# Performance work log

Hardware: AMD Instinct MI355X
Metric: run time of the kernel (lower is better)

## Reference

```python
import jax, jax.numpy as jnp
import numpy as np

B, N, C, K = 8, 4096, 64, 16
MLP = [64, 64, 128]
IN_CH = C * 2 + 3  # 131
EPS = 1e-5


def setup_inputs() -> dict:
    key = jax.random.key(0)
    ks = jax.random.split(key, 16)
    inp = {
        "pos1": jax.random.normal(ks[0], (B, 3, N), jnp.float32),
        "pos1_re": jax.random.normal(ks[1], (B, 3, N), jnp.float32),
        "pos2": jax.random.normal(ks[2], (B, 3, N), jnp.float32),
        "feature1": jax.random.normal(ks[3], (B, C, N), jnp.float32),
        "feature2": jax.random.normal(ks[4], (B, C, N), jnp.float32),
        "ksample": K,
    }
    # 1x1 Conv2d weights (out, in), no bias; BN affine params per layer
    last = IN_CH
    for i, out in enumerate(MLP):
        inp[f"W{i}"] = jax.random.normal(ks[5 + i], (out, last), jnp.float32) * (1.0 / np.sqrt(last))
        inp[f"g{i}"] = 1.0 + 0.1 * jax.random.normal(ks[8 + i], (out,), jnp.float32)
        inp[f"b{i}"] = 0.1 * jax.random.normal(ks[11 + i], (out,), jnp.float32)
        last = out
    return inp


def _knn_idx(query, ref, k):
    # query: [B,N,3], ref: [B,M,3] -> idx [B,N,k] of nearest refs per query
    q2 = jnp.sum(query * query, -1, keepdims=True)          # [B,N,1]
    r2 = jnp.sum(ref * ref, -1)[:, None, :]                 # [B,1,M]
    d = q2 + r2 - 2.0 * jnp.einsum("bnc,bmc->bnm", query, ref)
    _, idx = jax.lax.top_k(-d, k)
    return idx


def _group(x, idx):
    # x: [B,Cx,M], idx: [B,N,k] -> [B,Cx,N,k]
    xt = jnp.transpose(x, (0, 2, 1))                         # [B,M,Cx]
    g = jax.vmap(lambda a, i: a[i])(xt, idx)                 # [B,N,k,Cx]
    return jnp.transpose(g, (0, 3, 1, 2))


def _bn_relu(x, g, b):
    # training-mode BatchNorm2d over (B,N,k) per channel, then ReLU
    mean = jnp.mean(x, axis=(0, 2, 3), keepdims=True)
    var = jnp.mean((x - mean) ** 2, axis=(0, 2, 3), keepdims=True)
    xh = (x - mean) * jax.lax.rsqrt(var + EPS)
    return jax.nn.relu(xh * g[None, :, None, None] + b[None, :, None, None])


def reference(pos1, pos1_re, pos2, feature1, feature2, ksample,
              W0, g0, b0, W1, g1, b1, W2, g2, b2):
    idx = _knn_idx(jnp.transpose(pos1_re, (0, 2, 1)),
                   jnp.transpose(pos2, (0, 2, 1)), ksample)   # [B,N,k]
    pos2_g = _group(pos2, idx)                                # [B,3,N,k]
    pos_diff = pos2_g - pos1[:, :, :, None]
    feat2_g = _group(feature2, idx)                           # [B,C,N,k]
    feat1_rep = jnp.broadcast_to(feature1[:, :, :, None], feat2_g.shape)
    x = jnp.concatenate([pos_diff, feat2_g, feat1_rep], axis=1)  # [B,2C+3,N,k]
    for W, g, b in ((W0, g0, b0), (W1, g1, b1), (W2, g2, b2)):
        x = _bn_relu(jnp.einsum("oc,bcnk->bonk", W, x), g, b)
    feat1_new = jnp.max(x, axis=-1)                           # [B,mlp[-1],N]
    return pos1, feat1_new
```

## Files before the change

### kernel.cpp

```cpp
#include <hip/hip_runtime.h>
#include <hip/hip_bf16.h>
#include <cstdint>
#include <cstddef>

#define BB   8
#define NN   4096
#define CC   64
#define KK   16
#define H2   128
#define NPOSF 524288.0f
#define BNEPS 1e-5f

typedef __attribute__((ext_vector_type(8))) short  short8;
typedef __attribute__((ext_vector_type(4))) float  f32x4;

#define MFMA(a,b,c) __builtin_amdgcn_mfma_f32_16x16x32_bf16(a, b, c, 0, 0, 0)

__device__ __forceinline__ unsigned short f2bf(float x) {
  union { float f; unsigned u; } v; v.f = x;
  unsigned u = v.u;
  return (unsigned short)((u + 0x7fffu + ((u >> 16) & 1u)) >> 16);
}
__device__ __forceinline__ float bf2f(unsigned short h) {
  union { unsigned u; float f; } v; v.u = ((unsigned)h) << 16; return v.f;
}
__device__ __forceinline__ unsigned long long shflxor64(unsigned long long v, int j) {
  unsigned lo = (unsigned)v, hi = (unsigned)(v >> 32);
  lo = (unsigned)__shfl_xor((int)lo, j);
  hi = (unsigned)__shfl_xor((int)hi, j);
  return ((unsigned long long)hi << 32) | lo;
}
__device__ __forceinline__ unsigned long long shfl64(unsigned long long v, int src) {
  unsigned lo = (unsigned)v, hi = (unsigned)(v >> 32);
  lo = (unsigned)__shfl((int)lo, src);
  hi = (unsigned)__shfl((int)hi, src);
  return ((unsigned long long)hi << 32) | lo;
}

#define BN_INLINE(S_, Q_, g_, b_, aLds, bLds, CH) \
  if (t < CH) { \
    float s = 0.f, qq = 0.f; \
    for (int c = 0; c < 32; ++c) { s += S_[c*CH + t]; qq += Q_[c*CH + t]; } \
    float mean = s * (1.0f / NPOSF); \
    float var  = qq * (1.0f / NPOSF) - mean*mean; \
    float rs   = 1.0f / sqrtf(var + BNEPS); \
    float a    = g_[t] * rs; \
    aLds[t] = a; bLds[t] = b_[t] - mean*a; \
  }

__global__ __launch_bounds__(256) void k_prep(const float* __restrict__ pos2, float4* __restrict__ out,
                                              const float* __restrict__ pos1, float* __restrict__ outP,
                                              float* __restrict__ stats) {
  int i = blockIdx.x * 256 + threadIdx.x;
  int b = i >> 12, n = i & 4095;
  float x = pos2[(b*3 + 0)*NN + n];
  float y = pos2[(b*3 + 1)*NN + n];
  float z = pos2[(b*3 + 2)*NN + n];
  float w = __fadd_rn(__fadd_rn(__fmul_rn(x,x), __fmul_rn(y,y)), __fmul_rn(z,z));
  out[i] = make_float4(x, y, z, w);
  if (i < BB*3*NN/4) {
    *(float4*)(outP + i*4) = *(const float4*)(pos1 + i*4);
  }
  if (i < 16384) stats[i] = 0.f;
}

__global__ __launch_bounds__(256) void k_transposeb2(const float* __restrict__ f2, const float* __restrict__ f1,
                                                     unsigned short* __restrict__ o2, unsigned short* __restrict__ o1) {
  __shared__ float tile[32][33];
  int z = blockIdx.z;
  int b = z & 7;
  const float* in = (z < 8) ? f2 : f1;
  unsigned short* out = (z < 8) ? o2 : o1;
  int n0 = blockIdx.x * 32, c0 = blockIdx.y * 32;
  int tx = threadIdx.x, ty = threadIdx.y;
  #pragma unroll
  for (int i = 0; i < 32; i += 8)
    tile[ty + i][tx] = in[((size_t)(b*CC + c0 + ty + i))*NN + n0 + tx];
  __syncthreads();
  #pragma unroll
  for (int i = 0; i < 32; i += 8)
    out[((size_t)(b*NN + n0 + ty + i))*CC + c0 + tx] = f2bf(tile[tx][ty + i]);
}

__global__ __launch_bounds__(256) void k_wt(const float* __restrict__ W0, const float* __restrict__ W1,
                                            const float* __restrict__ W2, unsigned short* __restrict__ Apk0,
                                            unsigned short* __restrict__ Apk1, unsigned short* __restrict__ Apk2) {
  int i = blockIdx.x * 256 + threadIdx.x;
  if (i < 1280) {
    int mt = i / 320, r = i % 320, s = r / 64, lane = r % 64;
    int o = mt*16 + (lane & 15), q = lane >> 4, fi = mt*5 + s;
    #pragma unroll
    for (int j = 0; j < 8; ++j) {
      int c = s*32 + q*8 + j;
      float w = 0.f;
      if (c < 131) { int cs = (c < 128) ? (c + 3) : (c - 128); w = W0[o*131 + cs]; }
      Apk0[((size_t)(fi)*64 + lane)*8 + j] = f2bf(w);
    }
  } else if (i < 1792) {
    int k = i - 1280, mt = k / 128, r = k % 128, s = r / 64, lane = r % 64;
    int o = mt*16 + (lane & 15), q = lane >> 4, fi = mt*2 + s;
    #pragma unroll
    for (int j = 0; j < 8; ++j) {
      int c = s*32 + q*8 + j;
      Apk1[((size_t)(fi)*64 + lane)*8 + j] = f2bf(W1[o*64 + c]);
    }
  } else if (i < 2816) {
    int k = i - 1792, mt = k / 128, r = k % 128, s = r / 64, lane = r % 64;
    int o = mt*16 + (lane & 15), q = lane >> 4, fi = mt*2 + s;
    #pragma unroll
    for (int j = 0; j < 8; ++j) {
      int c = s*32 + q*8 + j;
      Apk2[((size_t)(fi)*64 + lane)*8 + j] = f2bf(W2[o*64 + c]);
    }
  }
}

__global__ __launch_bounds__(256) void k_packAB(const float* __restrict__ pos1_re,
                                                const float4* __restrict__ pos2t,
                                                unsigned short* __restrict__ ApkQ,
                                                unsigned short* __restrict__ BpkR) {
  int i = blockIdx.x * 256 + threadIdx.x;
  int half = i >> 17;
  int ii = i & 131071;
  int b = ii >> 14, r = ii & 16383;
  int qt = r >> 6, lane = r & 63;
  int li = lane & 15, g = lane >> 4;
  int n = qt*16 + li;
  if (half == 0) {
    float q[3];
    q[0] = pos1_re[(b*3 + 0)*NN + n];
    q[1] = pos1_re[(b*3 + 1)*NN + n];
    q[2] = pos1_re[(b*3 + 2)*NN + n];
    unsigned short qhi[3], qlo[3];
    #pragma unroll
    for (int c = 0; c < 3; ++c) {
      qhi[c] = f2bf(q[c]);
      qlo[c] = f2bf(__fsub_rn(q[c], bf2f(qhi[c])));
    }
    #pragma unroll
    for (int j = 0; j < 8; ++j) {
      int k = g*8 + j;
      unsigned short v = 0;
      if (k < 3)       v = qhi[k];
      else if (k < 6)  v = qhi[k-3];
      else if (k < 9)  v = qlo[k-6];
      else if (k < 11) v = 0x3F80;
      ApkQ[(((size_t)b*256 + qt)*64 + lane)*8 + j] = v;
    }
  } else {
    float4 rr = pos2t[(size_t)b*NN + n];
    float rc[3] = {rr.x, rr.y, rr.z};
    unsigned short m2hi[3], m2lo[3];
    #pragma unroll
    for (int c = 0; c < 3; ++c) {
      unsigned short rhi = f2bf(rc[c]);
      float rhif = bf2f(rhi);
      m2hi[c] = f2bf(-2.f * rhif);
      unsigned short rlo = f2bf(__fsub_rn(rc[c], rhif));
      m2lo[c] = f2bf(-2.f * bf2f(rlo));
    }
    float r2 = rr.w;
    unsigned short r2hi = f2bf(r2);
    unsigned short r2lo = f2bf(__fsub_rn(r2, bf2f(r2hi)));
    #pragma unroll
    for (int j = 0; j < 8; ++j) {
      int k = g*8 + j;
      unsigned short v = 0;
      if (k < 3)       v = m2hi[k];
      else if (k < 6)  v = m2lo[k-3];
      else if (k < 9)  v = m2hi[k-6];
      else if (k == 9) v = r2hi;
      else if (k == 10)v = r2lo;
      BpkR[(((size_t)b*256 + qt)*64 + lane)*8 + j] = v;
    }
  }
}

__global__ __launch_bounds__(512, 8) void k_knnf(const float* __restrict__ pos1_re,
                                                 const float4* __restrict__ pos2t,
                                                 const unsigned short* __restrict__ ApkQ,
                                                 const unsigned short* __restrict__ BpkR,
                                                 unsigned short* __restrict__ idxOut) {
  __shared__ unsigned short lists[16*128];
  __shared__ unsigned cnts[16];
  __shared__ float smin[16][128];
  __shared__ float thr[16][2];
  const int t = threadIdx.x, lane = t & 63, wv = t >> 6;
  const int b = blockIdx.y;
  const int qt = blockIdx.x;
  const int li = lane & 15, g = lane >> 4;

  if (t < 16) cnts[t] = 0;

  short8 af = *(const short8*)(ApkQ + (((size_t)b*256 + qt)*64 + lane)*8);
  const unsigned short* bq = BpkR + (size_t)b*256*512 + lane*8;

  const f32x4 zero4 = {0,0,0,0};

  float mn[4] = {3e38f, 3e38f, 3e38f, 3e38f};
  const int off = qt & 3;
  #pragma unroll
  for (int s = 0; s < 8; ++s) {
    short8 bf = *(const short8*)(bq + (size_t)(wv*32 + s*4 + off)*512);
    f32x4 a = MFMA(af, bf, zero4);
    #pragma unroll
    for (int rg = 0; rg < 4; ++rg) mn[rg] = fminf(mn[rg], a[rg]);
  }
  #pragma unroll
  for (int rg = 0; rg < 4; ++rg) smin[g*4 + rg][wv*16 + li] = mn[rg];
  __syncthreads();

  #pragma unroll 1
  for (int c = 0; c < 2; ++c) {
    const int rr = wv*2 + c;
    float v = fminf(smin[rr][lane], smin[rr][64 + lane]);
    #pragma unroll
    for (int k = 2; k <= 64; k <<= 1)
      #pragma unroll
      for (int j = k>>1; j > 0; j >>= 1) {
        float p = __shfl_xor(v, j);
        bool keepMin = (((lane & j) == 0) == ((lane & k) == 0));
        float mn_ = fminf(v, p), mx_ = fmaxf(v, p);
        v = keepMin ? mn_ : mx_;
      }
    float t10 = __shfl(v, 9);
    if (lane == 0) {
      const int n = qt*16 + rr;
      float qx = pos1_re[(b*3 + 0)*NN + n];
      float qy = pos1_re[(b*3 + 1)*NN + n];
      float qz = pos1_re[(b*3 + 2)*NN + n];
      float q2 = __fadd_rn(__fadd_rn(__fmul_rn(qx,qx), __fmul_rn(qy,qy)), __fmul_rn(qz,qz));
      float eps2 = __fmaf_rn(1.25e-4f, q2 + 64.f, 6e-4f);
      thr[rr][0] = t10;
      thr[rr][1] = t10 + eps2;
    }
  }
  __syncthreads();
  float tsr[4], twr[4];
  #pragma unroll
  for (int rg = 0; rg < 4; ++rg) { tsr[rg] = thr[g*4 + rg][0]; twr[rg] = thr[g*4 + rg][1]; }

  #pragma unroll 8
  for (int s = 0; s < 32; ++s) {
    const int rt = wv*32 + s;
    short8 bf = *(const short8*)(bq + (size_t)rt*512);
    f32x4 a = MFMA(af, bf, zero4);
    bool any = (a[0] < twr[0]) | (a[1] < twr[1]) | (a[2] < twr[2]) | (a[3] < twr[3]);
    if (__ballot(any)) {
      #pragma unroll
      for (int rg = 0; rg < 4; ++rg) {
        if (a[rg] < twr[rg]) {
          unsigned add = (a[rg] < tsr[rg]) ? 1u : 0x10001u;
          unsigned prev = atomicAdd(&cnts[g*4 + rg], add);
          unsigned pos = prev & 0xffffu;
          if (pos < 128u) lists[((g*4 + rg) << 7) | pos] = (unsigned short)((rt << 4) | li);
        }
      }
    }
  }
  __syncthreads();

  const float4* rp = pos2t + (size_t)b*NN;
  #pragma unroll 1
  for (int c = 0; c < 2; ++c) {
    const int qi = wv*2 + c;
    const int n = qt*16 + qi;
    unsigned cw = cnts[qi];
    unsigned cnt = cw & 0xffffu;
    int c0q = (int)cnt - (int)(cw >> 16);

    const float qx = pos1_re[(b*3 + 0)*NN + n];
    const float qy = pos1_re[(b*3 + 1)*NN + n];
    const float qz = pos1_re[(b*3 + 2)*NN + n];
    const float q2 = __fadd_rn(__fadd_rn(__fmul_rn(qx,qx), __fmul_rn(qy,qy)), __fmul_rn(qz,qz));

    if (c0q >= 16 && cnt <= 128u) {
      const unsigned short* lst = &lists[qi << 7];
      unsigned long long key = ~0ull;
      if (lane < (int)cnt) {
        int ix = lst[lane];
        float4 r = rp[ix];
        float dot = __fadd_rn(__fadd_rn(__fmul_rn(qx,r.x), __fmul_rn(qy,r.y)), __fmul_rn(qz,r.z));
        float d   = __fsub_rn(__fadd_rn(q2, r.w), __fmul_rn(2.0f, dot));
        unsigned du = __float_as_uint(d);
        du ^= (du >> 31) ? 0xFFFFFFFFu : 0x80000000u;
        key = ((unsigned long long)du << 16) | (unsigned)ix;
      }
      #pragma unroll
      for (int k = 2; k <= 64; k <<= 1)
        #pragma unroll
        for (int j = k>>1; j > 0; j >>= 1) {
          unsigned long long p = shflxor64(key, j);
          bool keepMin = (((lane & j) == 0) == ((lane & k) == 0));
          unsigned long long mnk = key < p ? key : p, mxk = key < p ? p : key;
          key = keepMin ? mnk : mxk;
        }
      if (cnt > 64u) {
        unsigned long long k2 = ~0ull;
        if (lane + 64 < (int)cnt) {
          int ix = lst[64 + lane];
          float4 r = rp[ix];
          float dot = __fadd_rn(__fadd_rn(__fmul_rn(qx,r.x), __fmul_rn(qy,r.y)), __fmul_rn(qz,r.z));
          float d   = __fsub_rn(__fadd_rn(q2, r.w), __fmul_rn(2.0f, dot));
          unsigned du = __float_as_uint(d);
          du ^= (du >> 31) ? 0xFFFFFFFFu : 0x80000000u;
          k2 = ((unsigned long long)du << 16) | (unsigned)ix;
        }
        #pragma unroll
        for (int k = 2; k <= 64; k <<= 1)
          #pragma unroll
          for (int j = k>>1; j > 0; j >>= 1) {
            unsigned long long p = shflxor64(k2, j);
            bool keepMin = (((lane & j) == 0) == ((lane & k) == 0));
            unsigned long long mnk = k2 < p ? k2 : p, mxk = k2 < p ? p : k2;
            k2 = keepMin ? mnk : mxk;
          }
        unsigned long long pb = shfl64(k2, (15 - lane) & 63);
        key = key < pb ? key : pb;
      }
      if (lane < 16) idxOut[((size_t)(b*NN + n))*KK + lane] = (unsigned short)(key & 0xffffull);
    } else {
      unsigned bd  = 0xFFFFFFFFu;
      unsigned bix = 0u;
      unsigned tau = 0xFFFFFFFFu;
      for (int it = 0; it < 64; ++it) {
        float4 r = rp[it*64 + lane];
        float dot = __fadd_rn(__fadd_rn(__fmul_rn(qx,r.x), __fmul_rn(qy,r.y)), __fmul_rn(qz,r.z));
        float d   = __fsub_rn(__fadd_rn(q2, r.w), __fmul_rn(2.0f, dot));
        unsigned du = __float_as_uint(d);
        du ^= (du >> 31) ? 0xFFFFFFFFu : 0x80000000u;
        unsigned long long mask = __ballot(du < tau);
        while (mask) {
          const int l = __ffsll((unsigned long long)mask) - 1;
          mask &= (mask - 1);
          const unsigned sd = (unsigned)__builtin_amdgcn_readlane((int)du, l);
          if (sd >= tau) continue;
          const unsigned sidx = (unsigned)(it*64 + l);
          int m = (bd > sd) ? 1 : 0;
          int pm = __builtin_amdgcn_update_dpp(0, m, 0x111, 0xF, 0xF, true);
          unsigned sb = (unsigned)__builtin_amdgcn_update_dpp(0, (int)bd,  0x111, 0xF, 0xF, true);
          unsigned si = (unsigned)__builtin_amdgcn_update_dpp(0, (int)bix, 0x111, 0xF, 0xF, true);
          if (m) { bd = pm ? sb : sd; bix = pm ? si : sidx; }
          tau = (unsigned)__builtin_amdgcn_readlane((int)bd, 15);
        }
      }
      if (lane < 16) idxOut[((size_t)(b*NN + n))*KK + lane] = (unsigned short)bix;
    }
  }
}

#define WAVE_STATS(NMT) { \
  _Pragma("unroll") \
  for (int mt = 0; mt < NMT; ++mt) { \
    _Pragma("unroll") \
    for (int rg = 0; rg < 4; ++rg) { \
      float s_ = sacc[mt][rg], q_ = sqacc[mt][rg]; \
      s_ += __shfl_xor(s_,1); s_ += __shfl_xor(s_,2); s_ += __shfl_xor(s_,4); s_ += __shfl_xor(s_,8); \
      q_ += __shfl_xor(q_,1); q_ += __shfl_xor(q_,2); q_ += __shfl_xor(q_,4); q_ += __shfl_xor(q_,8); \
      if (cl == 0) { atomicAdd(&sS[mt*16 + q*4 + rg], s_); atomicAdd(&sQ[mt*16 + q*4 + rg], q_); } \
    } \
  } }

__global__ __launch_bounds__(256) void k_layer0(
    const unsigned short* __restrict__ nidx, const float4* __restrict__ pos2t,
    const float* __restrict__ pos1, const unsigned short* __restrict__ f2b,
    const unsigned short* __restrict__ f1b, const unsigned short* __restrict__ Apk0,
    unsigned short* __restrict__ Y0, float* __restrict__ gS, float* __restrict__ gQ) {
  __shared__ float sS[64], sQ[64];
  const int t = threadIdx.x, lane = t & 63, wv = t >> 6;
  const int b = blockIdx.x & 7, xt = blockIdx.x >> 3;
  const int n0 = xt*32 + wv*8;
  const int cl = lane & 15, q = lane >> 4;

  short8 Wr[20];
  #pragma unroll
  for (int f = 0; f < 20; ++f) Wr[f] = *(const short8*)(Apk0 + ((size_t)f*64 + lane)*8);
  if (t < 64) { sS[t] = 0.f; sQ[t] = 0.f; }
  __syncthreads();

  f32x4 sacc[4]  = {{0,0,0,0},{0,0,0,0},{0,0,0,0},{0,0,0,0}};
  f32x4 sqacc[4] = {{0,0,0,0},{0,0,0,0},{0,0,0,0},{0,0,0,0}};

  #pragma unroll 1
  for (int p = 0; p < 8; ++p) {
    const int n = n0 + p;
    const int m = (int)nidx[((size_t)(b*NN + n))*KK + cl];
    const unsigned short* f2r = f2b + ((size_t)(b*NN + m))*64;
    const unsigned short* f1r = f1b + ((size_t)(b*NN + n))*64;
    short8 x0 = *(const short8*)(f2r + q*8);
    short8 x1 = *(const short8*)(f2r + 32 + q*8);
    short8 x2 = *(const short8*)(f1r + q*8);
    short8 x3 = *(const short8*)(f1r + 32 + q*8);
    short8 x4 = {0,0,0,0,0,0,0,0};
    if (q == 0) {
      float4 pp = pos2t[(size_t)b*NN + m];
      float px = pos1[(b*3 + 0)*NN + n];
      float py = pos1[(b*3 + 1)*NN + n];
      float pz = pos1[(b*3 + 2)*NN + n];
      x4[0] = (short)f2bf(pp.x - px);
      x4[1] = (short)f2bf(pp.y - py);
      x4[2] = (short)f2bf(pp.z - pz);
    }
    f32x4 acc[4] = {{0,0,0,0},{0,0,0,0},{0,0,0,0},{0,0,0,0}};
    #pragma unroll
    for (int mt = 0; mt < 4; ++mt) {
      acc[mt] = MFMA(Wr[mt*5 + 0], x0, acc[mt]);
      acc[mt] = MFMA(Wr[mt*5 + 1], x1, acc[mt]);
      acc[mt] = MFMA(Wr[mt*5 + 2], x2, acc[mt]);
      acc[mt] = MFMA(Wr[mt*5 + 3], x3, acc[mt]);
      acc[mt] = MFMA(Wr[mt*5 + 4], x4, acc[mt]);
    }
    unsigned short* yr = Y0 + (((size_t)(b*NN + n))*KK + cl)*64;
    #pragma unroll
    for (int mt = 0; mt < 4; ++mt) {
      sacc[mt]  += acc[mt];
      sqacc[mt] += acc[mt]*acc[mt];
      ushort4 pk; pk.x = f2bf(acc[mt][0]); pk.y = f2bf(acc[mt][1]);
      pk.z = f2bf(acc[mt][2]); pk.w = f2bf(acc[mt][3]);
      *(ushort4*)(yr + mt*16 + q*4) = pk;
    }
  }
  WAVE_STATS(4)
  __syncthreads();
  const int slot = xt & 31;
  if (t < 64) { atomicAdd(&gS[slot*64 + t], sS[t]); atomicAdd(&gQ[slot*64 + t], sQ[t]); }
}

__global__ __launch_bounds__(256) void k_layer1(
    const unsigned short* __restrict__ Y0, const float* __restrict__ S0, const float* __restrict__ Q0,
    const float* __restrict__ g0, const float* __restrict__ b0,
    const unsigned short* __restrict__ Apk1, unsigned short* __restrict__ Y1,
    float* __restrict__ gS, float* __restrict__ gQ) {
  __shared__ float sS[64], sQ[64];
  __shared__ float aL[64], bL[64];
  const int t = threadIdx.x, lane = t & 63, wv = t >> 6;
  const int b = blockIdx.y, n0 = blockIdx.x*32 + wv*8;
  const int cl = lane & 15, q = lane >> 4;

  short8 Wr[8];
  #pragma unroll
  for (int f = 0; f < 8; ++f) Wr[f] = *(const short8*)(Apk1 + ((size_t)f*64 + lane)*8);
  BN_INLINE(S0, Q0, g0, b0, aL, bL, 64)
  if (t >= 64 && t < 128) { sS[t-64] = 0.f; sQ[t-64] = 0.f; }
  __syncthreads();

  float ar[16], br[16];
  #pragma unroll
  for (int s = 0; s < 2; ++s)
    #pragma unroll
    for (int j = 0; j < 8; ++j) { int c = s*32 + q*8 + j; ar[s*8+j] = aL[c]; br[s*8+j] = bL[c]; }

  f32x4 sacc[4]  = {{0,0,0,0},{0,0,0,0},{0,0,0,0},{0,0,0,0}};
  f32x4 sqacc[4] = {{0,0,0,0},{0,0,0,0},{0,0,0,0},{0,0,0,0}};

  #pragma unroll 1
  for (int p = 0; p < 8; ++p) {
    const int n = n0 + p;
    const unsigned short* yr = Y0 + (((size_t)(b*NN + n))*KK + cl)*64;
    short8 u0 = *(const short8*)(yr + q*8);
    short8 u1 = *(const short8*)(yr + 32 + q*8);
    short8 x0, x1;
    #pragma unroll
    for (int j = 0; j < 8; ++j) {
      x0[j] = (short)f2bf(fmaxf(bf2f((unsigned short)u0[j])*ar[j]   + br[j],   0.f));
      x1[j] = (short)f2bf(fmaxf(bf2f((unsigned short)u1[j])*ar[8+j] + br[8+j], 0.f));
    }
    f32x4 acc[4] = {{0,0,0,0},{0,0,0,0},{0,0,0,0},{0,0,0,0}};
    #pragma unroll
    for (int mt = 0; mt < 4; ++mt) {
      acc[mt] = MFMA(Wr[mt*2 + 0], x0, acc[mt]);
      acc[mt] = MFMA(Wr[mt*2 + 1], x1, acc[mt]);
    }
    unsigned short* yw = Y1 + (((size_t)(b*NN + n))*KK + cl)*64;
    #pragma unroll
    for (int mt = 0; mt < 4; ++mt) {
      sacc[mt]  += acc[mt];
      sqacc[mt] += acc[mt]*acc[mt];
      ushort4 pk; pk.x = f2bf(acc[mt][0]); pk.y = f2bf(acc[mt][1]);
      pk.z = f2bf(acc[mt][2]); pk.w = f2bf(acc[mt][3]);
      *(ushort4*)(yw + mt*16 + q*4) = pk;
    }
  }
  WAVE_STATS(4)
  __syncthreads();
  const int slot = blockIdx.x & 31;
  if (t < 64) { atomicAdd(&gS[slot*64 + t], sS[t]); atomicAdd(&gQ[slot*64 + t], sQ[t]); }
}

__global__ __launch_bounds__(256) void k_l2stats(
    const unsigned short* __restrict__ Y1, const float* __restrict__ S1, const float* __restrict__ Q1,
    const float* __restrict__ g1, const float* __restrict__ b1,
    const unsigned short* __restrict__ Apk2, float2* __restrict__ Ypk,
    float* __restrict__ gS, float* __restrict__ gQ) {
  __shared__ float sS[128], sQ[128];
  __shared__ float aL[64], bL[64];
  const int t = threadIdx.x, lane = t & 63, wv = t >> 6;
  const int b = blockIdx.y, n0 = blockIdx.x*32 + wv*8;
  const int cl = lane & 15, q = lane >> 4;

  short8 Wr[16];
  #pragma unroll
  for (int f = 0; f < 16; ++f) Wr[f] = *(const short8*)(Apk2 + ((size_t)f*64 + lane)*8);
  BN_INLINE(S1, Q1, g1, b1, aL, bL, 64)
  if (t >= 64 && t < 192) { sS[t-64] = 0.f; sQ[t-64] = 0.f; }
  __syncthreads();

  float ar[16], br[16];
  #pragma unroll
  for (int s = 0; s < 2; ++s)
    #pragma unroll
    for (int j = 0; j < 8; ++j) { int c = s*32 + q*8 + j; ar[s*8+j] = aL[c]; br[s*8+j] = bL[c]; }

  float ssum[8] = {0,0,0,0,0,0,0,0};
  float sqsum[8] = {0,0,0,0,0,0,0,0};

  #pragma unroll 1
  for (int p = 0; p < 8; ++p) {
    const int n = n0 + p;
    const unsigned short* yr = Y1 + (((size_t)(b*NN + n))*KK + cl)*64;
    short8 u0 = *(const short8*)(yr + q*8);
    short8 u1 = *(const short8*)(yr + 32 + q*8);
    short8 x0, x1;
    #pragma unroll
    for (int j = 0; j < 8; ++j) {
      x0[j] = (short)f2bf(fmaxf(bf2f((unsigned short)u0[j])*ar[j]   + br[j],   0.f));
      x1[j] = (short)f2bf(fmaxf(bf2f((unsigned short)u1[j])*ar[8+j] + br[8+j], 0.f));
    }
    float2* yw = Ypk + ((size_t)(b*NN + n))*H2;
    #pragma unroll
    for (int mt = 0; mt < 8; ++mt) {
      f32x4 acc = {0,0,0,0};
      acc = MFMA(x0, Wr[mt*2 + 0], acc);
      acc = MFMA(x1, Wr[mt*2 + 1], acc);
      ssum[mt]  += (acc[0] + acc[1]) + (acc[2] + acc[3]);
      sqsum[mt] += acc[0]*acc[0] + acc[1]*acc[1] + acc[2]*acc[2] + acc[3]*acc[3];
      float mx = fmaxf(fmaxf(acc[0], acc[1]), fmaxf(acc[2], acc[3]));
      float mn = fminf(fminf(acc[0], acc[1]), fminf(acc[2], acc[3]));
      mx = fmaxf(mx, __shfl_xor(mx, 16)); mx = fmaxf(mx, __shfl_xor(mx, 32));
      mn = fminf(mn, __shfl_xor(mn, 16)); mn = fminf(mn, __shfl_xor(mn, 32));
      if (lane < 16) yw[mt*16 + lane] = make_float2(mx, mn);
    }
  }
  #pragma unroll
  for (int mt = 0; mt < 8; ++mt) {
    float s_ = ssum[mt], q_ = sqsum[mt];
    s_ += __shfl_xor(s_, 16); s_ += __shfl_xor(s_, 32);
    q_ += __shfl_xor(q_, 16); q_ += __shfl_xor(q_, 32);
    if (lane < 16) { atomicAdd(&sS[mt*16 + cl], s_); atomicAdd(&sQ[mt*16 + cl], q_); }
  }
  __syncthreads();
  const int slot = blockIdx.x & 31;
  if (t < 128) { atomicAdd(&gS[slot*128 + t], sS[t]); atomicAdd(&gQ[slot*128 + t], sQ[t]); }
}

__global__ __launch_bounds__(256) void k_bnmax(
    const float2* __restrict__ Ypk, const float* __restrict__ S2, const float* __restrict__ Q2,
    const float* __restrict__ g2, const float* __restrict__ b2,
    float* __restrict__ outF) {
  __shared__ float a2s[128], b2s[128];
  __shared__ float oBuf[32*128];
  const int t = threadIdx.x;
  const int b = blockIdx.y, nb = blockIdx.x*32;
  BN_INLINE(S2, Q2, g2, b2, a2s, b2s, 128)
  __syncthreads();

  const float2* src = Ypk + ((size_t)(b*NN + nb))*H2;
  #pragma unroll
  for (int e = 0; e < 16; ++e) {
    int i = e*256 + t;
    float2 v = src[i];
    int ch = i & 127;
    float a = a2s[ch];
    float sel = (a >= 0.f) ? v.x : v.y;
    oBuf[i] = fmaxf(sel*a + b2s[ch], 0.f);
  }
  __syncthreads();
  {
    const int ch = t & 127, npb = (t >> 7) * 16;
    #pragma unroll
    for (int g = 0; g < 4; ++g) {
      float4 v = make_float4(oBuf[(npb + g*4 + 0)*128 + ch],
                             oBuf[(npb + g*4 + 1)*128 + ch],
                             oBuf[(npb + g*4 + 2)*128 + ch],
                             oBuf[(npb + g*4 + 3)*128 + ch]);
      *(float4*)(outF + ((size_t)(b*H2 + ch))*NN + nb + npb + g*4) = v;
    }
  }
}

extern "C" void kernel_launch(void* const* d_in, const int* in_sizes, int n_in,
                              void* d_out, int out_size, void* d_ws, size_t ws_size,
                              hipStream_t stream) {
  const float* pos1    = (const float*)d_in[0];
  const float* pos1_re = (const float*)d_in[1];
  const float* pos2    = (const float*)d_in[2];
  const float* f1      = (const float*)d_in[3];
  const float* f2      = (const float*)d_in[4];
  const float* W0 = (const float*)d_in[6];
  const float* g0 = (const float*)d_in[7];
  const float* b0 = (const float*)d_in[8];
  const float* W1 = (const float*)d_in[9];
  const float* g1 = (const float*)d_in[10];
  const float* b1 = (const float*)d_in[11];
  const float* W2 = (const float*)d_in[12];
  const float* g2 = (const float*)d_in[13];
  const float* b2 = (const float*)d_in[14];
  float* out = (float*)d_out;

  char* ws = (char*)d_ws;
  float* stats = (float*)ws;
  float* S0 = stats;         float* Q0 = stats + 2048;
  float* S1 = stats + 4096;  float* Q1 = stats + 6144;
  float* S2 = stats + 8192;  float* Q2 = stats + 12288;
  unsigned short* Apk0 = (unsigned short*)(ws + 67584);
  unsigned short* Apk1 = (unsigned short*)(ws + 108544);
  unsigned short* Apk2 = (unsigned short*)(ws + 124928);
  unsigned short* idxb = (unsigned short*)(ws + 157696);
  float4* pos2t        = (float4*)(ws + 1206272);
  unsigned short* f2b  = (unsigned short*)(ws + 1730560);
  unsigned short* f1b  = (unsigned short*)(ws + 5924864);
  unsigned short* Y0   = (unsigned short*)(ws + 10119168);
  unsigned short* Y1   = (unsigned short*)(ws + 77228032);
  unsigned short* ApkQ = (unsigned short*)(ws + 10119168);
  unsigned short* BpkR = (unsigned short*)(ws + 10119168 + 2097152);
  float2* Ypk          = (float2*)(ws + 10119168);
  if (ws_size < 144336896u) return;

  k_wt<<<dim3(11), 256, 0, stream>>>(W0, W1, W2, Apk0, Apk1, Apk2);
  k_prep<<<dim3(BB*NN/256), 256, 0, stream>>>(pos2, pos2t, pos1, out, stats);
  k_packAB<<<dim3(1024), 256, 0, stream>>>(pos1_re, pos2t, ApkQ, BpkR);
  k_transposeb2<<<dim3(NN/32, CC/32, 2*BB), dim3(32, 8), 0, stream>>>(f2, f1, f2b, f1b);
  k_knnf<<<dim3(256, BB), 512, 0, stream>>>(pos1_re, pos2t, ApkQ, BpkR, idxb);

  k_layer0<<<dim3(NN/32*BB), 256, 0, stream>>>(idxb, pos2t, pos1, f2b, f1b, Apk0, Y0, S0, Q0);
  k_layer1<<<dim3(NN/32, BB), 256, 0, stream>>>(Y0, S0, Q0, g0, b0, Apk1, Y1, S1, Q1);
  k_l2stats<<<dim3(NN/32, BB), 256, 0, stream>>>(Y1, S1, Q1, g1, b1, Apk2, Ypk, S2, Q2);
  k_bnmax<<<dim3(NN/32, BB), 256, 0, stream>>>(Ypk, S2, Q2, g2, b2, out + (size_t)BB*3*NN);
}
```

Measured before the change: 310.6 us.

## Merge prep/pack kernels and interleave feature transpose blocks into kNN launch

Combines k_prep and k_packAB into one launch, with the pack half reading pos2 directly and recomputing the squared norm so it no longer depends on pos2t. The feature transpose work is folded into the kNN kernel as odd-numbered blocks, so the memory-bound transpose runs alongside the MFMA-heavy kNN blocks. This removes two kernel launches and their serialization gaps. In exchange the merged kNN kernel holds a shared union of LDS, and transpose blocks use 512 threads under a 512-thread launch bound.

```diff
diff --git a/kernel.cpp b/kernel.cpp
--- a/kernel.cpp
+++ b/kernel.cpp
@@ -48,78 +48,28 @@
     aLds[t] = a; bLds[t] = b_[t] - mean*a; \
   }
 
-__global__ __launch_bounds__(256) void k_prep(const float* __restrict__ pos2, float4* __restrict__ out,
-                                              const float* __restrict__ pos1, float* __restrict__ outP,
-                                              float* __restrict__ stats) {
-  int i = blockIdx.x * 256 + threadIdx.x;
-  int b = i >> 12, n = i & 4095;
-  float x = pos2[(b*3 + 0)*NN + n];
-  float y = pos2[(b*3 + 1)*NN + n];
-  float z = pos2[(b*3 + 2)*NN + n];
-  float w = __fadd_rn(__fadd_rn(__fmul_rn(x,x), __fmul_rn(y,y)), __fmul_rn(z,z));
-  out[i] = make_float4(x, y, z, w);
-  if (i < BB*3*NN/4) {
-    *(float4*)(outP + i*4) = *(const float4*)(pos1 + i*4);
-  }
-  if (i < 16384) stats[i] = 0.f;
-}
-
-__global__ __launch_bounds__(256) void k_transposeb2(const float* __restrict__ f2, const float* __restrict__ f1,
-                                                     unsigned short* __restrict__ o2, unsigned short* __restrict__ o1) {
-  __shared__ float tile[32][33];
-  int z = blockIdx.z;
-  int b = z & 7;
-  const float* in = (z < 8) ? f2 : f1;
-  unsigned short* out = (z < 8) ? o2 : o1;
-  int n0 = blockIdx.x * 32, c0 = blockIdx.y * 32;
-  int tx = threadIdx.x, ty = threadIdx.y;
-  #pragma unroll
-  for (int i = 0; i < 32; i += 8)
-    tile[ty + i][tx] = in[((size_t)(b*CC + c0 + ty + i))*NN + n0 + tx];
-  __syncthreads();
-  #pragma unroll
-  for (int i = 0; i < 32; i += 8)
-    out[((size_t)(b*NN + n0 + ty + i))*CC + c0 + tx] = f2bf(tile[tx][ty + i]);
-}
-
-__global__ __launch_bounds__(256) void k_wt(const float* __restrict__ W0, const float* __restrict__ W1,
-                                            const float* __restrict__ W2, unsigned short* __restrict__ Apk0,
-                                            unsigned short* __restrict__ Apk1, unsigned short* __restrict__ Apk2) {
-  int i = blockIdx.x * 256 + threadIdx.x;
-  if (i < 1280) {
-    int mt = i / 320, r = i % 320, s = r / 64, lane = r % 64;
-    int o = mt*16 + (lane & 15), q = lane >> 4, fi = mt*5 + s;
-    #pragma unroll
-    for (int j = 0; j < 8; ++j) {
-      int c = s*32 + q*8 + j;
-      float w = 0.f;
-      if (c < 131) { int cs = (c < 128) ? (c + 3) : (c - 128); w = W0[o*131 + cs]; }
-      Apk0[((size_t)(fi)*64 + lane)*8 + j] = f2bf(w);
-    }
-  } else if (i < 1792) {
-    int k = i - 1280, mt = k / 128, r = k % 128, s = r / 64, lane = r % 64;
-    int o = mt*16 + (lane & 15), q = lane >> 4, fi = mt*2 + s;
-    #pragma unroll
-    for (int j = 0; j < 8; ++j) {
-      int c = s*32 + q*8 + j;
-      Apk1[((size_t)(fi)*64 + lane)*8 + j] = f2bf(W1[o*64 + c]);
-    }
-  } else if (i < 2816) {
-    int k = i - 1792, mt = k / 128, r = k % 128, s = r / 64, lane = r % 64;
-    int o = mt*16 + (lane & 15), q = lane >> 4, fi = mt*2 + s;
-    #pragma unroll
-    for (int j = 0; j < 8; ++j) {
-      int c = s*32 + q*8 + j;
-      Apk2[((size_t)(fi)*64 + lane)*8 + j] = f2bf(W2[o*64 + c]);
-    }
-  }
-}
-
-__global__ __launch_bounds__(256) void k_packAB(const float* __restrict__ pos1_re,
-                                                const float4* __restrict__ pos2t,
-                                                unsigned short* __restrict__ ApkQ,
-                                                unsigned short* __restrict__ BpkR) {
-  int i = blockIdx.x * 256 + threadIdx.x;
+__global__ __launch_bounds__(256) void k_prep2(const float* __restrict__ pos2, float4* __restrict__ out,
+                                               const float* __restrict__ pos1, float* __restrict__ outP,
+                                               float* __restrict__ stats,
+                                               const float* __restrict__ pos1_re,
+                                               unsigned short* __restrict__ ApkQ,
+                                               unsigned short* __restrict__ BpkR) {
+  const int bid = blockIdx.x;
+  if (bid < 128) {
+    int i = bid * 256 + threadIdx.x;
+    int b = i >> 12, n = i & 4095;
+    float x = pos2[(b*3 + 0)*NN + n];
+    float y = pos2[(b*3 + 1)*NN + n];
+    float z = pos2[(b*3 + 2)*NN + n];
+    float w = __fadd_rn(__fadd_rn(__fmul_rn(x,x), __fmul_rn(y,y)), __fmul_rn(z,z));
+    out[i] = make_float4(x, y, z, w);
+    if (i < BB*3*NN/4) {
+      *(float4*)(outP + i*4) = *(const float4*)(pos1 + i*4);
+    }
+    if (i < 16384) stats[i] = 0.f;
+    return;
+  }
+  int i = (bid - 128) * 256 + threadIdx.x;
   int half = i >> 17;
   int ii = i & 131071;
   int b = ii >> 14, r = ii & 16383;
@@ -148,8 +98,11 @@
       ApkQ[(((size_t)b*256 + qt)*64 + lane)*8 + j] = v;
     }
   } else {
-    float4 rr = pos2t[(size_t)b*NN + n];
-    float rc[3] = {rr.x, rr.y, rr.z};
+    float rx = pos2[(b*3 + 0)*NN + n];
+    float ry = pos2[(b*3 + 1)*NN + n];
+    float rz = pos2[(b*3 + 2)*NN + n];
+    float r2 = __fadd_rn(__fadd_rn(__fmul_rn(rx,rx), __fmul_rn(ry,ry)), __fmul_rn(rz,rz));
+    float rc[3] = {rx, ry, rz};
     unsigned short m2hi[3], m2lo[3];
     #pragma unroll
     for (int c = 0; c < 3; ++c) {
@@ -159,7 +112,6 @@
       unsigned short rlo = f2bf(__fsub_rn(rc[c], rhif));
       m2lo[c] = f2bf(-2.f * bf2f(rlo));
     }
-    float r2 = rr.w;
     unsigned short r2hi = f2bf(r2);
     unsigned short r2lo = f2bf(__fsub_rn(r2, bf2f(r2hi)));
     #pragma unroll
@@ -176,18 +128,79 @@
   }
 }
 
-__global__ __launch_bounds__(512, 8) void k_knnf(const float* __restrict__ pos1_re,
+__global__ __launch_bounds__(256) void k_wt(const float* __restrict__ W0, const float* __restrict__ W1,
+                                            const float* __restrict__ W2, unsigned short* __restrict__ Apk0,
+                                            unsigned short* __restrict__ Apk1, unsigned short* __restrict__ Apk2) {
+  int i = blockIdx.x * 256 + threadIdx.x;
+  if (i < 1280) {
+    int mt = i / 320, r = i % 320, s = r / 64, lane = r % 64;
+    int o = mt*16 + (lane & 15), q = lane >> 4, fi = mt*5 + s;
+    #pragma unroll
+    for (int j = 0; j < 8; ++j) {
+      int c = s*32 + q*8 + j;
+      float w = 0.f;
+      if (c < 131) { int cs = (c < 128) ? (c + 3) : (c - 128); w = W0[o*131 + cs]; }
+      Apk0[((size_t)(fi)*64 + lane)*8 + j] = f2bf(w);
+    }
+  } else if (i < 1792) {
+    int k = i - 1280, mt = k / 128, r = k % 128, s = r / 64, lane = r % 64;
+    int o = mt*16 + (lane & 15), q = lane >> 4, fi = mt*2 + s;
+    #pragma unroll
+    for (int j = 0; j < 8; ++j) {
+      int c = s*32 + q*8 + j;
+      Apk1[((size_t)(fi)*64 + lane)*8 + j] = f2bf(W1[o*64 + c]);
+    }
+  } else if (i < 2816) {
+    int k = i - 1792, mt = k / 128, r = k % 128, s = r / 64, lane = r % 64;
+    int o = mt*16 + (lane & 15), q = lane >> 4, fi = mt*2 + s;
+    #pragma unroll
+    for (int j = 0; j < 8; ++j) {
+      int c = s*32 + q*8 + j;
+      Apk2[((size_t)(fi)*64 + lane)*8 + j] = f2bf(W2[o*64 + c]);
+    }
+  }
+}
+
+__global__ __launch_bounds__(512, 8) void k_knnt(const float* __restrict__ pos1_re,
                                                  const float4* __restrict__ pos2t,
                                                  const unsigned short* __restrict__ ApkQ,
                                                  const unsigned short* __restrict__ BpkR,
-                                                 unsigned short* __restrict__ idxOut) {
-  __shared__ unsigned short lists[16*128];
-  __shared__ unsigned cnts[16];
-  __shared__ float smin[16][128];
-  __shared__ float thr[16][2];
-  const int t = threadIdx.x, lane = t & 63, wv = t >> 6;
-  const int b = blockIdx.y;
-  const int qt = blockIdx.x;
+                                                 unsigned short* __restrict__ idxOut,
+                                                 const float* __restrict__ f2, const float* __restrict__ f1,
+                                                 unsigned short* __restrict__ o2, unsigned short* __restrict__ o1) {
+  __shared__ __align__(16) char smem[12544];
+  const int bid = blockIdx.x;
+  const int t = threadIdx.x;
+
+  if (bid & 1) {
+    const int sub = t >> 8, tt = t & 255;
+    const int tx = tt & 31, ty = tt >> 5;
+    const int L = (bid >> 1)*2 + sub;
+    const int xg = L & 127, yz = L >> 7;
+    const int yg = yz & 1, zg = yz >> 1;
+    const int b = zg & 7;
+    const float* in = (zg < 8) ? f2 : f1;
+    unsigned short* outp = (zg < 8) ? o2 : o1;
+    const int n0 = xg * 32, c0 = yg * 32;
+    float (*tile)[33] = (float(*)[33])(smem + sub*4224);
+    #pragma unroll
+    for (int i = 0; i < 32; i += 8)
+      tile[ty + i][tx] = in[((size_t)(b*CC + c0 + ty + i))*NN + n0 + tx];
+    __syncthreads();
+    #pragma unroll
+    for (int i = 0; i < 32; i += 8)
+      outp[((size_t)(b*NN + n0 + ty + i))*CC + c0 + tx] = f2bf(tile[tx][ty + i]);
+    return;
+  }
+
+  unsigned short* lists = (unsigned short*)smem;
+  unsigned* cnts        = (unsigned*)(smem + 4096);
+  float (*smin)[128]    = (float(*)[128])(smem + 4160);
+  float (*thr)[2]       = (float(*)[2])(smem + 12352);
+  const int kb = bid >> 1;
+  const int lane = t & 63, wv = t >> 6;
+  const int b = kb >> 8;
+  const int qt = kb & 255;
   const int li = lane & 15, g = lane >> 4;
 
   if (t < 16) cnts[t] = 0;
@@ -627,10 +640,8 @@
   if (ws_size < 144336896u) return;
 
   k_wt<<<dim3(11), 256, 0, stream>>>(W0, W1, W2, Apk0, Apk1, Apk2);
-  k_prep<<<dim3(BB*NN/256), 256, 0, stream>>>(pos2, pos2t, pos1, out, stats);
-  k_packAB<<<dim3(1024), 256, 0, stream>>>(pos1_re, pos2t, ApkQ, BpkR);
-  k_transposeb2<<<dim3(NN/32, CC/32, 2*BB), dim3(32, 8), 0, stream>>>(f2, f1, f2b, f1b);
-  k_knnf<<<dim3(256, BB), 512, 0, stream>>>(pos1_re, pos2t, ApkQ, BpkR, idxb);
+  k_prep2<<<dim3(1152), 256, 0, stream>>>(pos2, pos2t, pos1, out, stats, pos1_re, ApkQ, BpkR);
+  k_knnt<<<dim3(4096), 512, 0, stream>>>(pos1_re, pos2t, ApkQ, BpkR, idxb, f2, f1, f2b, f1b);
 
   k_layer0<<<dim3(NN/32*BB), 256, 0, stream>>>(idxb, pos2t, pos1, f2b, f1b, Apk0, Y0, S0, Q0);
   k_layer1<<<dim3(NN/32, BB), 256, 0, stream>>>(Y0, S0, Q0, g0, b0, Apk1, Y1, S1, Q1);
```

After: 350.3 us. 1.13x slower.
